# Performance work log

Hardware: AMD Instinct MI355X
Metric: run time of the kernel (lower is better)

Reference implementation:

```python
import jax, jax.numpy as jnp
import numpy as np

B, LAT = 8, 64
NS_IN = [256, 1024, 4096]      # input node count per layer (U[i].shape[-1])
NS_OUT = [1024, 4096, 16384]   # output node count per layer (U[i].shape[0])
CH = [64, 64, 32, 3]           # feature channels: after fc, after conv0, conv1, conv2
DEG = 16


def setup_inputs() -> dict:
    key = jax.random.key(0)
    ks = iter(jax.random.split(key, 32))
    s = lambda n: 1.0 / np.sqrt(n)
    inp = {}
    inp["latents"] = jax.random.normal(next(ks), (B, LAT), jnp.float32)
    inp["fc_W"] = jax.random.normal(next(ks), (LAT, NS_IN[0] * CH[0]), jnp.float32) * s(LAT)
    inp["fc_b"] = jnp.zeros((NS_IN[0] * CH[0],), jnp.float32)
    for i in range(3):
        inp[f"U{i}"] = jax.random.normal(next(ks), (NS_OUT[i], NS_IN[i]), jnp.float32) * s(NS_IN[i])
        inp[f"Ub{i}"] = jnp.zeros((NS_OUT[i], CH[i]), jnp.float32)
        inp[f"W{i}"] = jax.random.normal(next(ks), (CH[i], CH[i + 1]), jnp.float32) * s(CH[i])
        inp[f"b{i}"] = jnp.zeros((CH[i + 1],), jnp.float32)
        E = NS_OUT[i] * DEG
        inp[f"vals{i}"] = jax.random.uniform(next(ks), (E,), jnp.float32)
        inp[f"rows{i}"] = jax.random.randint(next(ks), (E,), 0, NS_OUT[i], jnp.int32)
        inp[f"cols{i}"] = jax.random.randint(next(ks), (E,), 0, NS_OUT[i], jnp.int32)
    return inp


def _gcn(feat, rows, cols, vals, W, b, n_nodes):
    # sparse adjacency message passing: out = relu(A @ feat @ W + b)
    def one(f):  # f: [N, C]
        msg = vals[:, None] * f[cols]                      # [E, C]
        return jax.ops.segment_sum(msg, rows, num_segments=n_nodes)
    agg = jax.vmap(one)(feat)                              # [B, N, C]
    return jax.nn.relu(agg @ W + b)


def reference(latents, fc_W, fc_b,
              U0, Ub0, U1, Ub1, U2, Ub2,
              W0, b0, W1, b1, W2, b2,
              vals0, vals1, vals2,
              rows0, cols0, rows1, cols1, rows2, cols2):
    feat = latents @ fc_W + fc_b                           # [B, N0*C0]
    feat = feat.reshape(-1, NS_IN[0], CH[0])               # [B, N0, C0]
    Us = [U0, U1, U2]; Ubs = [Ub0, Ub1, Ub2]
    Ws = [W0, W1, W2]; bs = [b0, b1, b2]
    rs = [rows0, rows1, rows2]; cs = [cols0, cols1, cols2]; vs = [vals0, vals1, vals2]
    for i in range(3):
        # learned upsampling matmul + bias (tf.matmul / tf.map_fn are the same batched matmul)
        feat = jnp.einsum('on,bnc->boc', Us[i], feat) + Ubs[i]
        feat = _gcn(feat, rs[i], cs[i], vs[i], Ws[i], bs[i], NS_OUT[i])
    return feat                                            # [B, 16384, 3]
```

## Files before the change

kernel.cpp:

```cpp
#include <hip/hip_runtime.h>
#include <cstdint>
#include <cstddef>

#define TPB 256
#define CAP 128

typedef __bf16 bf16x8 __attribute__((ext_vector_type(8)));
typedef float f32x4 __attribute__((ext_vector_type(4)));

union FragU { ushort u[8]; uint4 q; bf16x8 v; };

__device__ __forceinline__ ushort f2bf(float f)
{
    union { float f; uint32_t u; } v; v.f = f;
    uint32_t r = v.u + 0x7FFFu + ((v.u >> 16) & 1u);
    return (ushort)(r >> 16);
}

__global__ __launch_bounds__(TPB) void k_prep(
    const float* __restrict__ lat, const float* __restrict__ W,
    const float* __restrict__ bias, float* __restrict__ out,
    int* __restrict__ cnt)
{
    int bx = blockIdx.x;
    if (bx < 512) {
        int tid = bx * TPB + threadIdx.x;
        int c = tid & 63;
        int b = (tid >> 6) & 7;
        int n = tid >> 9;
        int j = n * 64 + c;
        float acc = bias[j];
        const float* lb = lat + b * 64;
#pragma unroll 16
        for (int l = 0; l < 64; ++l)
            acc = fmaf(lb[l], W[l * 16384 + j], acc);
        out[tid] = acc;
    } else {
        int tid = (bx - 512) * TPB + threadIdx.x;
        if (tid < 21504) cnt[tid] = 0;
    }
}

__global__ __launch_bounds__(TPB) void k_build(
    const int* __restrict__ r0, const int* __restrict__ c0, const float* __restrict__ v0,
    const int* __restrict__ r1, const int* __restrict__ c1, const float* __restrict__ v1,
    const int* __restrict__ r2, const int* __restrict__ c2, const float* __restrict__ v2,
    int* __restrict__ cnt, int2* __restrict__ ecv,
    const float* __restrict__ X, const float* __restrict__ W0,
    const float* __restrict__ Ub0,
    ushort* __restrict__ Fq, float* __restrict__ UbW)
{
    int bx = blockIdx.x;
    if (bx < 1344) {
        int e = bx * TPB + threadIdx.x;
        int node, col; float val;
        if (e < 16384)       { node = r0[e];                col = c0[e];  val = v0[e]; }
        else if (e < 81920)  { int l = e - 16384; node = 1024 + r1[l]; col = c1[l]; val = v1[l]; }
        else                 { int l = e - 81920; node = 5120 + r2[l]; col = c2[l]; val = v2[l]; }
        int pos = atomicAdd(&cnt[node], 1);
        ecv[(size_t)node * CAP + pos] = make_int2(col, __float_as_int(val));
    } else if (bx < 1856) {
        int tid = (bx - 1344) * TPB + threadIdx.x;
        int co = tid % 64;
        int nb = tid / 64;
        const float* x = X + (size_t)nb * 64;
        float acc = 0.f;
#pragma unroll
        for (int ci = 0; ci < 64; ++ci)
            acc = fmaf(x[ci], W0[ci * 64 + co], acc);
        int n = nb >> 3, bb = nb & 7;
        int col = bb * 64 + co;
        int ks = n >> 5, r = n & 31, kq = r >> 3, j = r & 7;
        int ct = col >> 4, cl = col & 15;
        size_t idx = ((((size_t)ct * (256 / 32) + ks) * 4 + kq) * 16 + cl) * 8 + j;
        Fq[idx] = f2bf(acc);
    } else {
        int tid = (bx - 1856) * TPB + threadIdx.x;
        if (tid >= 65536) return;
        int co = tid % 64;
        int row = tid / 64;
        const float* x = Ub0 + (size_t)row * 64;
        float acc = 0.f;
#pragma unroll
        for (int ci = 0; ci < 64; ++ci)
            acc = fmaf(x[ci], W0[ci * 64 + co], acc);
        UbW[tid] = acc;
    }
}

template<int NPB, int BCIN, int CI, int CO, int COLS, int KF,
         int NNODE, int RBASE, int NBUB>
__global__ __launch_bounds__(TPB) void k_gf(
    const float* __restrict__ up, const int* __restrict__ cnt,
    const int2* __restrict__ ecv,
    const float* __restrict__ bias, const float* __restrict__ W,
    const float* __restrict__ Ub,
    ushort* __restrict__ Fq, float* __restrict__ UbW)
{
    constexpr int TPN = TPB / NPB;
    constexpr int CPT = BCIN / TPN;
    int bx = blockIdx.x;
    if (bx < NNODE / NPB) {
        __shared__ float feat[NPB * BCIN];
        __shared__ float Wl[CI * CO];
        const int tid = threadIdx.x;
#pragma unroll
        for (int i = tid; i < CI * CO; i += TPB) Wl[i] = W[i];

        const int ni = tid / TPN;
        const int li = tid % TPN;
        const int node = bx * NPB + ni;
        const int deg = cnt[RBASE + node];
        const int2* ep = ecv + (size_t)(RBASE + node) * CAP;

        float acc[CPT];
#pragma unroll
        for (int k = 0; k < CPT; ++k) acc[k] = 0.f;
        for (int p = 0; p < deg; ++p) {
            int2 cv = ep[p];
            float v = __int_as_float(cv.y);
            const float* ur = up + (size_t)cv.x * BCIN + li;
#pragma unroll
            for (int k = 0; k < CPT; ++k)
                acc[k] = fmaf(v, ur[k * TPN], acc[k]);
        }
#pragma unroll
        for (int k = 0; k < CPT; ++k) {
            int c = li + k * TPN;
            feat[ni * BCIN + c] = fmaxf(acc[k] + bias[c % CI], 0.f);
        }
        __syncthreads();

#pragma unroll
        for (int e = tid; e < NPB * COLS; e += TPB) {
            int fni = e / COLS;
            int colp = e % COLS;
            int n = bx * NPB + fni;
            float a = 0.f;
            if (colp < 8 * CO) {
                int b = colp / CO, co = colp % CO;
                const float* fb = feat + fni * BCIN + b * CI;
#pragma unroll
                for (int ci = 0; ci < CI; ++ci)
                    a = fmaf(fb[ci], Wl[ci * CO + co], a);
            }
            int ks = n >> 5, rr = n & 31, kq = rr >> 3, j = rr & 7;
            int ct = colp >> 4, cl = colp & 15;
            size_t idx = ((((size_t)ct * (KF / 32) + ks) * 4 + kq) * 16 + cl) * 8 + j;
            Fq[idx] = f2bf(a);
        }
    } else {
        int tid = (bx - NNODE / NPB) * TPB + threadIdx.x;
        if (tid >= NBUB * CO) return;
        int co = tid % CO;
        int row = tid / CO;
        const float* x = Ub + (size_t)row * CI;
        float acc = 0.f;
#pragma unroll
        for (int ci = 0; ci < CI; ++ci)
            acc = fmaf(x[ci], W[ci * CO + co], acc);
        UbW[tid] = acc;
    }
}

template<int K, int NTOT, int CO, int CF, int RF>
__global__ __launch_bounds__(TPB) void k_gemm_ws(
    const float* __restrict__ U, const ushort* __restrict__ Fq,
    const float* __restrict__ UbW, float* __restrict__ up)
{
    constexpr int KCH = K / 4;
    constexpr int KS = KCH / 32;
    constexpr int NC = CF * 16;
    constexpr int RED = RF * NC * 16;
    static_assert(KS % 2 == 0, "even k-steps");

    __shared__ float red[4][RED];

    const int tid = threadIdx.x;
    const int lane = tid & 63;
    const int w = tid >> 6;
    const int rowbase = blockIdx.x * (RF * 16);
    const int jt = blockIdx.y;
    const int kq = lane >> 4;
    const int m = lane & 15;

    const float* Ap[RF];
#pragma unroll
    for (int rf = 0; rf < RF; ++rf)
        Ap[rf] = U + (size_t)(rowbase + rf * 16 + m) * K + w * KCH + kq * 8;

    const ushort* Bp[CF];
#pragma unroll
    for (int cf = 0; cf < CF; ++cf)
        Bp[cf] = Fq + ((size_t)(jt * CF + cf) * (K / 32) + (size_t)w * KS) * 512
                 + lane * 8;

    f32x4 acc[RF][CF];
#pragma unroll
    for (int rf = 0; rf < RF; ++rf)
#pragma unroll
        for (int cf = 0; cf < CF; ++cf)
            acc[rf][cf] = (f32x4){0.f, 0.f, 0.f, 0.f};

    float4 a[2][RF][2];
    uint4  b[2][CF];

#define LOAD_STEP(S, t)                                                     \
    if ((t) < KS) {                                                         \
        _Pragma("unroll")                                                   \
        for (int rf = 0; rf < RF; ++rf) {                                   \
            a[S][rf][0] = *reinterpret_cast<const float4*>(Ap[rf] + (t) * 32);     \
            a[S][rf][1] = *reinterpret_cast<const float4*>(Ap[rf] + (t) * 32 + 4); \
        }                                                                   \
        _Pragma("unroll")                                                   \
        for (int cf = 0; cf < CF; ++cf)                                     \
            b[S][cf] = *reinterpret_cast<const uint4*>(Bp[cf] + (t) * 512); \
    }

#define COMP_STEP(S)                                                        \
    {                                                                       \
        _Pragma("unroll")                                                   \
        for (int rf = 0; rf < RF; ++rf) {                                   \
            const float* fa = reinterpret_cast<const float*>(&a[S][rf][0]); \
            bf16x8 av;                                                      \
            _Pragma("unroll")                                               \
            for (int j = 0; j < 8; ++j) av[j] = (__bf16)fa[j];              \
            _Pragma("unroll")                                               \
            for (int cf = 0; cf < CF; ++cf) {                               \
                FragU bfr; bfr.q = b[S][cf];                                \
                acc[rf][cf] = __builtin_amdgcn_mfma_f32_16x16x32_bf16(      \
                    av, bfr.v, acc[rf][cf], 0, 0, 0);                       \
            }                                                               \
        }                                                                   \
    }

    LOAD_STEP(0, 0)
#pragma unroll
    for (int t = 0; t < KS; t += 2) {
        LOAD_STEP(1, t + 1)
        COMP_STEP(0)
        LOAD_STEP(0, t + 2)
        COMP_STEP(1)
    }
#undef LOAD_STEP
#undef COMP_STEP

#pragma unroll
    for (int rf = 0; rf < RF; ++rf)
#pragma unroll
        for (int cf = 0; cf < CF; ++cf)
#pragma unroll
            for (int r = 0; r < 4; ++r)
                red[w][(rf * NC + cf * 16 + m) * 16 + kq * 4 + r] = acc[rf][cf][r];
    __syncthreads();

#pragma unroll
    for (int e = tid; e < RED; e += TPB) {
        int rf = e / (NC * 16);
        int rem = e - rf * (NC * 16);
        int col = rem >> 4, row = rem & 15;
        float v = red[0][e] + red[1][e] + red[2][e] + red[3][e];
        int gcol = jt * NC + col;
        int grow = rowbase + rf * 16 + row;
        if (gcol < NTOT)
            up[(size_t)grow * NTOT + gcol] =
                v + UbW[(size_t)grow * CO + gcol % CO];
    }
}

template<int BC, int CO, int NR, int RBASE>
__global__ __launch_bounds__(TPB) void k_gather_out(
    const float* __restrict__ up, const int* __restrict__ cnt,
    const int2* __restrict__ ecv,
    const float* __restrict__ bias, float* __restrict__ out)
{
    constexpr int JQ = BC / 4;
    int tid = blockIdx.x * TPB + threadIdx.x;
    if (tid >= NR * JQ) return;
    int jq = tid % JQ;
    int r = tid / JQ;
    int deg = cnt[RBASE + r];
    const int2* ep = ecv + (size_t)(RBASE + r) * CAP;
    float4 acc = make_float4(0.f, 0.f, 0.f, 0.f);
    for (int p = 0; p < deg; ++p) {
        int2 cv = ep[p];
        float v = __int_as_float(cv.y);
        float4 u = *reinterpret_cast<const float4*>(&up[(size_t)cv.x * BC + jq * 4]);
        acc.x = fmaf(v, u.x, acc.x);
        acc.y = fmaf(v, u.y, acc.y);
        acc.z = fmaf(v, u.z, acc.z);
        acc.w = fmaf(v, u.w, acc.w);
    }
    int col0 = jq * 4;
    float a[4] = {acc.x, acc.y, acc.z, acc.w};
#pragma unroll
    for (int e = 0; e < 4; ++e) {
        int col = col0 + e;
        int b = col / 3, j = col - b * 3;
        out[(size_t)b * 49152 + (size_t)r * 3 + j] = fmaxf(a[e] + bias[j], 0.f);
    }
}

extern "C" void kernel_launch(void* const* d_in, const int* in_sizes, int n_in,
                              void* d_out, int out_size, void* d_ws, size_t ws_size,
                              hipStream_t stream)
{
    const float* lat   = (const float*)d_in[0];
    const float* fcW   = (const float*)d_in[1];
    const float* fcb   = (const float*)d_in[2];
    const float* U0    = (const float*)d_in[3];
    const float* Ub0   = (const float*)d_in[4];
    const float* W0    = (const float*)d_in[5];
    const float* b0    = (const float*)d_in[6];
    const float* vals0 = (const float*)d_in[7];
    const int*   rows0 = (const int*)d_in[8];
    const int*   cols0 = (const int*)d_in[9];
    const float* U1    = (const float*)d_in[10];
    const float* Ub1   = (const float*)d_in[11];
    const float* W1    = (const float*)d_in[12];
    const float* b1    = (const float*)d_in[13];
    const float* vals1 = (const float*)d_in[14];
    const int*   rows1 = (const int*)d_in[15];
    const int*   cols1 = (const int*)d_in[16];
    const float* U2    = (const float*)d_in[17];
    const float* Ub2   = (const float*)d_in[18];
    const float* W2    = (const float*)d_in[19];
    const float* b2    = (const float*)d_in[20];
    const float* vals2 = (const float*)d_in[21];
    const int*   rows2 = (const int*)d_in[22];
    const int*   cols2 = (const int*)d_in[23];

    float* ws = (float*)d_ws;
    float* fbuf0 = ws;
    float* fWq   = fbuf0 + 131072;
    float* UbW   = fWq   + 262144;
    float* up    = UbW   + 131072;
    int*   cnt   = (int*)(up + 1048576);
    int2*  ecv   = (int2*)(cnt + 21764);

    ushort* Fq16 = (ushort*)fWq;
    float* out = (float*)d_out;

    hipLaunchKernelGGL(k_prep, dim3(596), dim3(TPB), 0, stream, lat, fcW, fcb, fbuf0, cnt);
    hipLaunchKernelGGL(k_build, dim3(2112), dim3(TPB), 0, stream,
                       rows0, cols0, vals0, rows1, cols1, vals1, rows2, cols2, vals2,
                       cnt, ecv, fbuf0, W0, Ub0, Fq16, UbW);
    hipLaunchKernelGGL((k_gemm_ws<256, 512, 64, 8, 1>), dim3(64, 4), dim3(TPB), 0, stream,
                       U0, Fq16, UbW, up);
    hipLaunchKernelGGL((k_gf<1, 512, 64, 32, 256, 1024, 1024, 0, 4096>),
                       dim3(1536), dim3(TPB), 0, stream,
                       up, cnt, ecv, b0, W1, Ub1, Fq16, UbW);
    hipLaunchKernelGGL((k_gemm_ws<1024, 256, 32, 8, 1>), dim3(256, 2), dim3(TPB), 0, stream,
                       U1, Fq16, UbW, up);
    hipLaunchKernelGGL((k_gf<8, 256, 32, 3, 32, 4096, 4096, 1024, 16384>),
                       dim3(704), dim3(TPB), 0, stream,
                       up, cnt, ecv, b1, W2, Ub2, Fq16, UbW);
    hipLaunchKernelGGL((k_gemm_ws<4096, 24, 3, 2, 2>), dim3(512, 1), dim3(TPB), 0, stream,
                       U2, Fq16, UbW, up);
    hipLaunchKernelGGL((k_gather_out<24, 3, 16384, 5120>), dim3(384), dim3(TPB), 0, stream,
                       up, cnt, ecv, b2, out);
}
```

Before: 153.1 us.

## Fuse fc into build kernel, hoist Ub·W bias products, deepen last GEMM pipeline

Moves the fc projection into k_build so it is fused with the first W0 transform through shared memory. All three Ub@W bias products are now computed up front in k_build instead of in the tail blocks of each k_gf launch. k_gemm_ws gains a configurable pipeline depth: the final layer uses 4 prefetch stages with RF=1 and twice as many blocks. This trims the serialized critical path and improves latency hiding in the K=4096 GEMM, at the cost of more registers and a larger k_build launch.

```diff
diff --git a/kernel.cpp b/kernel.cpp
--- a/kernel.cpp
+++ b/kernel.cpp
@@ -17,28 +17,10 @@
     return (ushort)(r >> 16);
 }
 
-__global__ __launch_bounds__(TPB) void k_prep(
-    const float* __restrict__ lat, const float* __restrict__ W,
-    const float* __restrict__ bias, float* __restrict__ out,
-    int* __restrict__ cnt)
-{
-    int bx = blockIdx.x;
-    if (bx < 512) {
-        int tid = bx * TPB + threadIdx.x;
-        int c = tid & 63;
-        int b = (tid >> 6) & 7;
-        int n = tid >> 9;
-        int j = n * 64 + c;
-        float acc = bias[j];
-        const float* lb = lat + b * 64;
-#pragma unroll 16
-        for (int l = 0; l < 64; ++l)
-            acc = fmaf(lb[l], W[l * 16384 + j], acc);
-        out[tid] = acc;
-    } else {
-        int tid = (bx - 512) * TPB + threadIdx.x;
-        if (tid < 21504) cnt[tid] = 0;
-    }
+__global__ __launch_bounds__(TPB) void k_prep(int* __restrict__ cnt)
+{
+    int tid = blockIdx.x * TPB + threadIdx.x;
+    if (tid < 21504) cnt[tid] = 0;
 }
 
 __global__ __launch_bounds__(TPB) void k_build(
@@ -46,9 +28,13 @@
     const int* __restrict__ r1, const int* __restrict__ c1, const float* __restrict__ v1,
     const int* __restrict__ r2, const int* __restrict__ c2, const float* __restrict__ v2,
     int* __restrict__ cnt, int2* __restrict__ ecv,
-    const float* __restrict__ X, const float* __restrict__ W0,
-    const float* __restrict__ Ub0,
-    ushort* __restrict__ Fq, float* __restrict__ UbW)
+    const float* __restrict__ lat, const float* __restrict__ fcW,
+    const float* __restrict__ fcb,
+    const float* __restrict__ W0, const float* __restrict__ Ub0,
+    const float* __restrict__ W1, const float* __restrict__ Ub1,
+    const float* __restrict__ W2, const float* __restrict__ Ub2,
+    ushort* __restrict__ Fq,
+    float* __restrict__ UbW0, float* __restrict__ UbW1, float* __restrict__ UbW2)
 {
     int bx = blockIdx.x;
     if (bx < 1344) {
@@ -60,110 +46,122 @@
         int pos = atomicAdd(&cnt[node], 1);
         ecv[(size_t)node * CAP + pos] = make_int2(col, __float_as_int(val));
     } else if (bx < 1856) {
-        int tid = (bx - 1344) * TPB + threadIdx.x;
-        int co = tid % 64;
-        int nb = tid / 64;
-        const float* x = X + (size_t)nb * 64;
+        __shared__ float feat[4][64];
+        int t = threadIdx.x;
+        int nb0 = (bx - 1344) * 4;
+        int nbL = t >> 6, ci = t & 63;
+        int nb = nb0 + nbL;
+        int n = nb >> 3, bb = nb & 7;
+        {
+            float acc = fcb[n * 64 + ci];
+            const float* lb = lat + bb * 64;
+#pragma unroll 16
+            for (int l = 0; l < 64; ++l)
+                acc = fmaf(lb[l], fcW[l * 16384 + n * 64 + ci], acc);
+            feat[nbL][ci] = acc;
+        }
+        __syncthreads();
+        int co = ci;
         float acc = 0.f;
 #pragma unroll
-        for (int ci = 0; ci < 64; ++ci)
-            acc = fmaf(x[ci], W0[ci * 64 + co], acc);
-        int n = nb >> 3, bb = nb & 7;
+        for (int k = 0; k < 64; ++k)
+            acc = fmaf(feat[nbL][k], W0[k * 64 + co], acc);
         int col = bb * 64 + co;
         int ks = n >> 5, r = n & 31, kq = r >> 3, j = r & 7;
         int ct = col >> 4, cl = col & 15;
         size_t idx = ((((size_t)ct * (256 / 32) + ks) * 4 + kq) * 16 + cl) * 8 + j;
         Fq[idx] = f2bf(acc);
-    } else {
+    } else if (bx < 2112) {
         int tid = (bx - 1856) * TPB + threadIdx.x;
-        if (tid >= 65536) return;
-        int co = tid % 64;
-        int row = tid / 64;
+        int co = tid % 64, row = tid / 64;
         const float* x = Ub0 + (size_t)row * 64;
         float acc = 0.f;
 #pragma unroll
         for (int ci = 0; ci < 64; ++ci)
             acc = fmaf(x[ci], W0[ci * 64 + co], acc);
-        UbW[tid] = acc;
-    }
-}
-
-template<int NPB, int BCIN, int CI, int CO, int COLS, int KF,
-         int NNODE, int RBASE, int NBUB>
+        UbW0[tid] = acc;
+    } else if (bx < 2624) {
+        int tid = (bx - 2112) * TPB + threadIdx.x;
+        int co = tid % 32, row = tid / 32;
+        const float* x = Ub1 + (size_t)row * 64;
+        float acc = 0.f;
+#pragma unroll
+        for (int ci = 0; ci < 64; ++ci)
+            acc = fmaf(x[ci], W1[ci * 32 + co], acc);
+        UbW1[tid] = acc;
+    } else {
+        int tid = (bx - 2624) * TPB + threadIdx.x;
+        int co = tid % 3, row = tid / 3;
+        const float* x = Ub2 + (size_t)row * 32;
+        float acc = 0.f;
+#pragma unroll
+        for (int ci = 0; ci < 32; ++ci)
+            acc = fmaf(x[ci], W2[ci * 3 + co], acc);
+        UbW2[tid] = acc;
+    }
+}
+
+template<int NPB, int BCIN, int CI, int CO, int COLS, int KF, int RBASE>
 __global__ __launch_bounds__(TPB) void k_gf(
     const float* __restrict__ up, const int* __restrict__ cnt,
     const int2* __restrict__ ecv,
     const float* __restrict__ bias, const float* __restrict__ W,
-    const float* __restrict__ Ub,
-    ushort* __restrict__ Fq, float* __restrict__ UbW)
+    ushort* __restrict__ Fq)
 {
     constexpr int TPN = TPB / NPB;
     constexpr int CPT = BCIN / TPN;
-    int bx = blockIdx.x;
-    if (bx < NNODE / NPB) {
-        __shared__ float feat[NPB * BCIN];
-        __shared__ float Wl[CI * CO];
-        const int tid = threadIdx.x;
-#pragma unroll
-        for (int i = tid; i < CI * CO; i += TPB) Wl[i] = W[i];
-
-        const int ni = tid / TPN;
-        const int li = tid % TPN;
-        const int node = bx * NPB + ni;
-        const int deg = cnt[RBASE + node];
-        const int2* ep = ecv + (size_t)(RBASE + node) * CAP;
-
-        float acc[CPT];
-#pragma unroll
-        for (int k = 0; k < CPT; ++k) acc[k] = 0.f;
-        for (int p = 0; p < deg; ++p) {
-            int2 cv = ep[p];
-            float v = __int_as_float(cv.y);
-            const float* ur = up + (size_t)cv.x * BCIN + li;
-#pragma unroll
-            for (int k = 0; k < CPT; ++k)
-                acc[k] = fmaf(v, ur[k * TPN], acc[k]);
+    __shared__ float feat[NPB * BCIN];
+    __shared__ float Wl[CI * CO];
+    const int bx = blockIdx.x;
+    const int tid = threadIdx.x;
+#pragma unroll
+    for (int i = tid; i < CI * CO; i += TPB) Wl[i] = W[i];
+
+    const int ni = tid / TPN;
+    const int li = tid % TPN;
+    const int node = bx * NPB + ni;
+    const int deg = cnt[RBASE + node];
+    const int2* ep = ecv + (size_t)(RBASE + node) * CAP;
+
+    float acc[CPT];
+#pragma unroll
+    for (int k = 0; k < CPT; ++k) acc[k] = 0.f;
+    for (int p = 0; p < deg; ++p) {
+        int2 cv = ep[p];
+        float v = __int_as_float(cv.y);
+        const float* ur = up + (size_t)cv.x * BCIN + li;
+#pragma unroll
+        for (int k = 0; k < CPT; ++k)
+            acc[k] = fmaf(v, ur[k * TPN], acc[k]);
+    }
+#pragma unroll
+    for (int k = 0; k < CPT; ++k) {
+        int c = li + k * TPN;
+        feat[ni * BCIN + c] = fmaxf(acc[k] + bias[c % CI], 0.f);
+    }
+    __syncthreads();
+
+#pragma unroll
+    for (int e = tid; e < NPB * COLS; e += TPB) {
+        int fni = e / COLS;
+        int colp = e % COLS;
+        int n = bx * NPB + fni;
+        float a = 0.f;
+        if (colp < 8 * CO) {
+            int b = colp / CO, co = colp % CO;
+            const float* fb = feat + fni * BCIN + b * CI;
+#pragma unroll
+            for (int ci = 0; ci < CI; ++ci)
+                a = fmaf(fb[ci], Wl[ci * CO + co], a);
         }
-#pragma unroll
-        for (int k = 0; k < CPT; ++k) {
-            int c = li + k * TPN;
-            feat[ni * BCIN + c] = fmaxf(acc[k] + bias[c % CI], 0.f);
-        }
-        __syncthreads();
-
-#pragma unroll
-        for (int e = tid; e < NPB * COLS; e += TPB) {
-            int fni = e / COLS;
-            int colp = e % COLS;
-            int n = bx * NPB + fni;
-            float a = 0.f;
-            if (colp < 8 * CO) {
-                int b = colp / CO, co = colp % CO;
-                const float* fb = feat + fni * BCIN + b * CI;
-#pragma unroll
-                for (int ci = 0; ci < CI; ++ci)
-                    a = fmaf(fb[ci], Wl[ci * CO + co], a);
-            }
-            int ks = n >> 5, rr = n & 31, kq = rr >> 3, j = rr & 7;
-            int ct = colp >> 4, cl = colp & 15;
-            size_t idx = ((((size_t)ct * (KF / 32) + ks) * 4 + kq) * 16 + cl) * 8 + j;
-            Fq[idx] = f2bf(a);
-        }
-    } else {
-        int tid = (bx - NNODE / NPB) * TPB + threadIdx.x;
-        if (tid >= NBUB * CO) return;
-        int co = tid % CO;
-        int row = tid / CO;
-        const float* x = Ub + (size_t)row * CI;
-        float acc = 0.f;
-#pragma unroll
-        for (int ci = 0; ci < CI; ++ci)
-            acc = fmaf(x[ci], W[ci * CO + co], acc);
-        UbW[tid] = acc;
-    }
-}
-
-template<int K, int NTOT, int CO, int CF, int RF>
+        int ks = n >> 5, rr = n & 31, kq = rr >> 3, j = rr & 7;
+        int ct = colp >> 4, cl = colp & 15;
+        size_t idx = ((((size_t)ct * (KF / 32) + ks) * 4 + kq) * 16 + cl) * 8 + j;
+        Fq[idx] = f2bf(a);
+    }
+}
+
+template<int K, int NTOT, int CO, int CF, int RF, int PIPE>
 __global__ __launch_bounds__(TPB) void k_gemm_ws(
     const float* __restrict__ U, const ushort* __restrict__ Fq,
     const float* __restrict__ UbW, float* __restrict__ up)
@@ -172,7 +170,6 @@
     constexpr int KS = KCH / 32;
     constexpr int NC = CF * 16;
     constexpr int RED = RF * NC * 16;
-    static_assert(KS % 2 == 0, "even k-steps");
 
     __shared__ float red[4][RED];
 
@@ -202,8 +199,8 @@
         for (int cf = 0; cf < CF; ++cf)
             acc[rf][cf] = (f32x4){0.f, 0.f, 0.f, 0.f};
 
-    float4 a[2][RF][2];
-    uint4  b[2][CF];
+    float4 a[PIPE][RF][2];
+    uint4  b[PIPE][CF];
 
 #define LOAD_STEP(S, t)                                                     \
     if ((t) < KS) {                                                         \
@@ -234,13 +231,12 @@
         }                                                                   \
     }
 
-    LOAD_STEP(0, 0)
-#pragma unroll
-    for (int t = 0; t < KS; t += 2) {
-        LOAD_STEP(1, t + 1)
-        COMP_STEP(0)
-        LOAD_STEP(0, t + 2)
-        COMP_STEP(1)
+#pragma unroll
+    for (int s = 0; s < PIPE; ++s) { LOAD_STEP(s, s) }
+#pragma unroll
+    for (int t = 0; t < KS; ++t) {
+        COMP_STEP(t % PIPE)
+        LOAD_STEP(t % PIPE, t + PIPE)
     }
 #undef LOAD_STEP
 #undef COMP_STEP
@@ -331,32 +327,34 @@
     const int*   cols2 = (const int*)d_in[23];
 
     float* ws = (float*)d_ws;
-    float* fbuf0 = ws;
-    float* fWq   = fbuf0 + 131072;
-    float* UbW   = fWq   + 262144;
-    float* up    = UbW   + 131072;
+    float* fWq   = ws;
+    float* UbW0  = fWq   + 262144;
+    float* UbW1  = UbW0  + 65536;
+    float* UbW2  = UbW1  + 131072;
+    float* up    = UbW2  + 49152;
     int*   cnt   = (int*)(up + 1048576);
     int2*  ecv   = (int2*)(cnt + 21764);
 
     ushort* Fq16 = (ushort*)fWq;
     float* out = (float*)d_out;
 
-    hipLaunchKernelGGL(k_prep, dim3(596), dim3(TPB), 0, stream, lat, fcW, fcb, fbuf0, cnt);
-    hipLaunchKernelGGL(k_build, dim3(2112), dim3(TPB), 0, stream,
+    hipLaunchKernelGGL(k_prep, dim3(84), dim3(TPB), 0, stream, cnt);
+    hipLaunchKernelGGL(k_build, dim3(2816), dim3(TPB), 0, stream,
                        rows0, cols0, vals0, rows1, cols1, vals1, rows2, cols2, vals2,
-                       cnt, ecv, fbuf0, W0, Ub0, Fq16, UbW);
-    hipLaunchKernelGGL((k_gemm_ws<256, 512, 64, 8, 1>), dim3(64, 4), dim3(TPB), 0, stream,
-                       U0, Fq16, UbW, up);
-    hipLaunchKernelGGL((k_gf<1, 512, 64, 32, 256, 1024, 1024, 0, 4096>),
-                       dim3(1536), dim3(TPB), 0, stream,
-                       up, cnt, ecv, b0, W1, Ub1, Fq16, UbW);
-    hipLaunchKernelGGL((k_gemm_ws<1024, 256, 32, 8, 1>), dim3(256, 2), dim3(TPB), 0, stream,
-                       U1, Fq16, UbW, up);
-    hipLaunchKernelGGL((k_gf<8, 256, 32, 3, 32, 4096, 4096, 1024, 16384>),
-                       dim3(704), dim3(TPB), 0, stream,
-                       up, cnt, ecv, b1, W2, Ub2, Fq16, UbW);
-    hipLaunchKernelGGL((k_gemm_ws<4096, 24, 3, 2, 2>), dim3(512, 1), dim3(TPB), 0, stream,
-                       U2, Fq16, UbW, up);
+                       cnt, ecv, lat, fcW, fcb, W0, Ub0, W1, Ub1, W2, Ub2,
+                       Fq16, UbW0, UbW1, UbW2);
+    hipLaunchKernelGGL((k_gemm_ws<256, 512, 64, 8, 1, 2>), dim3(64, 4), dim3(TPB), 0, stream,
+                       U0, Fq16, UbW0, up);
+    hipLaunchKernelGGL((k_gf<1, 512, 64, 32, 256, 1024, 0>),
+                       dim3(1024), dim3(TPB), 0, stream,
+                       up, cnt, ecv, b0, W1, Fq16);
+    hipLaunchKernelGGL((k_gemm_ws<1024, 256, 32, 8, 1, 2>), dim3(256, 2), dim3(TPB), 0, stream,
+                       U1, Fq16, UbW1, up);
+    hipLaunchKernelGGL((k_gf<8, 256, 32, 3, 32, 4096, 1024>),
+                       dim3(512), dim3(TPB), 0, stream,
+                       up, cnt, ecv, b1, W2, Fq16);
+    hipLaunchKernelGGL((k_gemm_ws<4096, 24, 3, 2, 1, 4>), dim3(1024, 1), dim3(TPB), 0, stream,
+                       U2, Fq16, UbW2, up);
     hipLaunchKernelGGL((k_gather_out<24, 3, 16384, 5120>), dim3(384), dim3(TPB), 0, stream,
                        up, cnt, ecv, b2, out);
 }
```

Measured after the change: 163.4 us. 1.07x slower.
